# Optimization experiments

Measured on AMD Instinct MI355X. Metric: run time of the kernel, lower is better.

## Reference

```python
import jax, jax.numpy as jnp
import numpy as np

N_HEADS = 8
NEG_INF = -1e9


def setup_inputs() -> dict:
    key = jax.random.key(0)
    ks = jax.random.split(key, 9)
    B, S, D = 4, 2048, 512
    scale = 1.0 / np.sqrt(D)
    x = jax.random.normal(ks[0], (B, S, D), dtype=jnp.float32)
    mask = jnp.tril(jnp.ones((S, S), dtype=bool))[None, None, :, :]  # causal [1,1,S,S]
    W_Q_w = jax.random.normal(ks[1], (D, D), dtype=jnp.float32) * scale
    W_Q_b = jax.random.normal(ks[2], (D,), dtype=jnp.float32) * 0.02
    W_K_w = jax.random.normal(ks[3], (D, D), dtype=jnp.float32) * scale
    W_K_b = jax.random.normal(ks[4], (D,), dtype=jnp.float32) * 0.02
    W_V_w = jax.random.normal(ks[5], (D, D), dtype=jnp.float32) * scale
    W_V_b = jax.random.normal(ks[6], (D,), dtype=jnp.float32) * 0.02
    W_O_w = jax.random.normal(ks[7], (D, D), dtype=jnp.float32) * scale
    W_O_b = jax.random.normal(ks[8], (D,), dtype=jnp.float32) * 0.02
    return {"x": x, "mask": mask,
            "W_Q_w": W_Q_w, "W_Q_b": W_Q_b, "W_K_w": W_K_w, "W_K_b": W_K_b,
            "W_V_w": W_V_w, "W_V_b": W_V_b, "W_O_w": W_O_w, "W_O_b": W_O_b}


def reference(x, mask, W_Q_w, W_Q_b, W_K_w, W_K_b, W_V_w, W_V_b, W_O_w, W_O_b):
    B, S, D = x.shape
    H = N_HEADS
    Dh = D // H
    # projections (torch Linear: x @ W.T + b), split heads -> [B,H,S,Dh]
    def split_heads(t):
        return t.reshape(B, S, H, Dh).transpose(0, 2, 1, 3)
    Q = split_heads(x @ W_Q_w.T + W_Q_b)
    K = split_heads(x @ W_K_w.T + W_K_b)
    V = split_heads(x @ W_V_w.T + W_V_b)
    # scaled dot-product attention with explicit [B,H,S,S] scores
    scores = jnp.einsum("bhqd,bhkd->bhqk", Q, K) / jnp.sqrt(jnp.float32(Dh))
    scores = jnp.where(mask, scores, jnp.float32(NEG_INF))
    att = jax.nn.softmax(scores, axis=-1)
    out = jnp.einsum("bhqk,bhkd->bhqd", att, V)
    out = out.transpose(0, 2, 1, 3).reshape(B, S, D)
    return out @ W_O_w.T + W_O_b
```

## Files before the change

kernel.cpp:

```cpp
#include <hip/hip_runtime.h>
#include <hip/hip_bf16.h>

#define BATCH 4
#define SEQ   2048
#define DIM   512
#define NH    8
#define DH    64
#define NTOK  (BATCH*SEQ)

typedef __bf16 bf16x8 __attribute__((ext_vector_type(8)));
typedef __bf16 bf16x4 __attribute__((ext_vector_type(4)));
typedef float  f32x4  __attribute__((ext_vector_type(4)));

#define MFMA16(a,b,c) __builtin_amdgcn_mfma_f32_16x16x32_bf16((a),(b),(c),0,0,0)

__device__ __forceinline__ void async_ld16(const __bf16* g, __bf16* l) {
  __builtin_amdgcn_global_load_lds(
      (const __attribute__((address_space(1))) void*)g,
      (__attribute__((address_space(3))) void*)l, 16, 0, 0);
}

__global__ __launch_bounds__(256) void cvt_all(
    const float* __restrict__ x,
    const float* __restrict__ s0, const float* __restrict__ s1,
    const float* __restrict__ s2, const float* __restrict__ s3,
    __bf16* __restrict__ xb,
    __bf16* __restrict__ o0, __bf16* __restrict__ o1,
    __bf16* __restrict__ o2, __bf16* __restrict__ o3) {
  int i = blockIdx.x * blockDim.x + threadIdx.x;
  const float* src;
  __bf16* dst;
  int off;
  if (i < NTOK*DIM/8) {
    src = x; dst = xb; off = i;
  } else {
    int w = i - NTOK*DIM/8;
    const int which = w >> 15;
    off = w & 32767;
    src = (which == 0) ? s0 : (which == 1) ? s1 : (which == 2) ? s2 : s3;
    dst = (which == 0) ? o0 : (which == 1) ? o1 : (which == 2) ? o2 : o3;
  }
  const float4* s = (const float4*)src;
  float4 a = s[2*off], b = s[2*off+1];
  bf16x8 o;
  o[0] = (__bf16)a.x; o[1] = (__bf16)a.y; o[2] = (__bf16)a.z; o[3] = (__bf16)a.w;
  o[4] = (__bf16)b.x; o[5] = (__bf16)b.y; o[6] = (__bf16)b.z; o[7] = (__bf16)b.w;
  *(bf16x8*)&dst[8*off] = o;
}

__global__ __launch_bounds__(256) void gemm_qkv(
    const __bf16* __restrict__ xb,
    const __bf16* __restrict__ wq, const __bf16* __restrict__ wk,
    const __bf16* __restrict__ wv,
    const float* __restrict__ bq, const float* __restrict__ bk,
    const float* __restrict__ bv,
    __bf16* __restrict__ Qb, __bf16* __restrict__ Kb, __bf16* __restrict__ Vt)
{
  const int z = blockIdx.z;
  const __bf16* W    = (z == 0) ? wq : (z == 1) ? wk : wv;
  const float*  bias = (z == 0) ? bq : (z == 1) ? bk : bv;

  __shared__ __bf16 S[2][128*64];
  __bf16* As = S[0];
  __bf16* Bs = S[1];

  const int tid  = threadIdx.x;
  const int m0   = blockIdx.x * 128, n0 = blockIdx.y * 128;
  const int w    = tid >> 6, lane = tid & 63, quad = lane >> 4, l16 = lane & 15;
  const int wm   = (w >> 1) * 64, wn = (w & 1) * 64;
  const int lrow = lane >> 3;
  const int lcol = (lane & 7) * 8;

  f32x4 acc[4][4] = {};

  const __bf16* Ag = xb + (size_t)m0 * DIM;
  const __bf16* Bg = W  + (size_t)n0 * DIM;

  for (int k0 = 0; k0 < DIM; k0 += 64) {
#pragma unroll
    for (int i = 0; i < 4; ++i) {
      const int rb = w*32 + i*8;
      async_ld16(&Ag[(size_t)(rb + lrow)*DIM + k0 + lcol], &As[rb*64]);
      async_ld16(&Bg[(size_t)(rb + lrow)*DIM + k0 + lcol], &Bs[rb*64]);
    }
    __syncthreads();
#pragma unroll
    for (int kk = 0; kk < 2; ++kk) {
      const int ko = kk*32 + quad*8;
      bf16x8 af[4], bfr[4];
#pragma unroll
      for (int f = 0; f < 4; ++f) {
        af[f]  = *(const bf16x8*)&As[(wm + f*16 + l16)*64 + ko];
        bfr[f] = *(const bf16x8*)&Bs[(wn + f*16 + l16)*64 + ko];
      }
#pragma unroll
      for (int fm = 0; fm < 4; ++fm)
#pragma unroll
        for (int fn = 0; fn < 4; ++fn)
          acc[fm][fn] = MFMA16(af[fm], bfr[fn], acc[fm][fn]);
    }
    __syncthreads();
  }

  __bf16* Cs = &S[0][0];
  if (z < 2) {
#pragma unroll
    for (int fm = 0; fm < 4; ++fm)
#pragma unroll
      for (int fn = 0; fn < 4; ++fn) {
        const int col = wn + fn*16 + l16;
        const float bc = bias[n0 + col];
        const int chunk = col >> 3, ce = col & 7;
#pragma unroll
        for (int r = 0; r < 4; ++r) {
          const int row = wm + fm*16 + quad*4 + r;
          Cs[row*128 + ((chunk ^ (row & 7)) << 3) + ce] = (__bf16)(acc[fm][fn][r] + bc);
        }
      }
  } else {
#pragma unroll
    for (int fm = 0; fm < 4; ++fm)
#pragma unroll
      for (int fn = 0; fn < 4; ++fn) {
        const int dhcol = wn + fn*16 + l16;
        const float bc = bias[n0 + dhcol];
        const int sbase = wm + fm*16 + quad*4;
        const int schunk = sbase >> 3, so = sbase & 7;
        __bf16* p = &Cs[dhcol*128 + ((schunk ^ (dhcol & 7)) << 3) + so];
#pragma unroll
        for (int r = 0; r < 4; ++r)
          p[r] = (__bf16)(acc[fm][fn][r] + bc);
      }
  }
  __syncthreads();
  {
    const int row = tid >> 1, half = tid & 1;
    if (z < 2) {
      __bf16* O = (z == 0) ? Qb : Kb;
      const int s = m0 + row, bb = s >> 11, ss = s & 2047;
#pragma unroll
      for (int j = 0; j < 8; ++j) {
        const int chunk = half*8 + j;
        bf16x8 v = *(const bf16x8*)&Cs[row*128 + ((chunk ^ (row & 7)) << 3)];
        const int colg = n0 + chunk*8;
        const int hh = colg >> 6, dh = colg & 63;
        *(bf16x8*)&O[((size_t)(bb*NH + hh)*SEQ + ss)*DH + dh] = v;
      }
    } else {
      const int colg = n0 + row;
      const int hh = colg >> 6, dh = colg & 63;
      const int bb = m0 >> 11, s0s = m0 & 2047;
#pragma unroll
      for (int j = 0; j < 8; ++j) {
        const int chunk = half*8 + j;
        bf16x8 v = *(const bf16x8*)&Cs[row*128 + ((chunk ^ (row & 7)) << 3)];
        *(bf16x8*)&Vt[((size_t)(bb*NH + hh)*DH + dh)*SEQ + s0s + chunk*8] = v;
      }
    }
  }
}

__global__ __launch_bounds__(256) void gemm_out(
    const __bf16* __restrict__ attnb, const __bf16* __restrict__ wo,
    const float* __restrict__ bo, float* __restrict__ out)
{
  __shared__ __bf16 S[2][128*64];
  __bf16* As = S[0];
  __bf16* Bs = S[1];

  const int tid = threadIdx.x;
  const int m0  = blockIdx.x * 128, n0 = blockIdx.y * 128;
  const int w   = tid >> 6, lane = tid & 63, quad = lane >> 4, l16 = lane & 15;
  const int wm  = (w >> 1) * 64, wn = (w & 1) * 64;
  const int lrow = lane >> 3, lcol = (lane & 7) * 8;

  f32x4 acc[4][4] = {};

  const __bf16* Ag = attnb + (size_t)m0 * DIM;
  const __bf16* Bg = wo    + (size_t)n0 * DIM;

  for (int k0 = 0; k0 < DIM; k0 += 64) {
#pragma unroll
    for (int i = 0; i < 4; ++i) {
      const int rb = w*32 + i*8;
      async_ld16(&Ag[(size_t)(rb + lrow)*DIM + k0 + lcol], &As[rb*64]);
      async_ld16(&Bg[(size_t)(rb + lrow)*DIM + k0 + lcol], &Bs[rb*64]);
    }
    __syncthreads();
#pragma unroll
    for (int kk = 0; kk < 2; ++kk) {
      const int ko = kk*32 + quad*8;
      bf16x8 af[4], bfr[4];
#pragma unroll
      for (int f = 0; f < 4; ++f) {
        af[f]  = *(const bf16x8*)&As[(wm + f*16 + l16)*64 + ko];
        bfr[f] = *(const bf16x8*)&Bs[(wn + f*16 + l16)*64 + ko];
      }
#pragma unroll
      for (int fm = 0; fm < 4; ++fm)
#pragma unroll
        for (int fn = 0; fn < 4; ++fn)
          acc[fm][fn] = MFMA16(af[fm], bfr[fn], acc[fm][fn]);
    }
    __syncthreads();
  }

#pragma unroll
  for (int fm = 0; fm < 4; ++fm) {
#pragma unroll
    for (int fn = 0; fn < 4; ++fn) {
      const int col  = n0 + wn + fn*16 + l16;
      const float bc = bo[col];
#pragma unroll
      for (int r = 0; r < 4; ++r) {
        const int row = m0 + wm + fm*16 + quad*4 + r;
        out[(size_t)row*DIM + col] = acc[fm][fn][r] + bc;
      }
    }
  }
}

__global__ __launch_bounds__(64) void flash_attn(
    const __bf16* __restrict__ Qb, const __bf16* __restrict__ Kb,
    const __bf16* __restrict__ Vt, __bf16* __restrict__ attnb)
{
  const int idx = blockIdx.x;
  const int bh  = idx & 31;
  const int qt  = 63 - (idx >> 5);
  const int b   = bh >> 3, h = bh & 7;
  const int lane = threadIdx.x & 63, quad = lane >> 4, l16 = lane & 15;
  const int q0  = qt * 32;

  const __bf16* Qp = Qb + (size_t)bh * SEQ * DH;
  const __bf16* Kp = Kb + (size_t)bh * SEQ * DH;
  const __bf16* Vp = Vt + (size_t)bh * DH * SEQ;

  __shared__ __bf16 Pt[32*72];

  bf16x8 qf[2][2];
#pragma unroll
  for (int nf = 0; nf < 2; ++nf)
#pragma unroll
    for (int kc = 0; kc < 2; ++kc) {
      bf16x8 q = *(const bf16x8*)&Qp[(size_t)(q0 + nf*16 + l16)*DH + kc*32 + quad*8];
#pragma unroll
      for (int j = 0; j < 8; ++j) q[j] = (__bf16)((float)q[j] * 0.125f);
      qf[nf][kc] = q;
    }

  f32x4 o[4][2] = {};
  float m_[2] = {-1e30f, -1e30f}, l_[2] = {0.f, 0.f};

  const int nt = (q0 >> 6) + 1;

  bf16x8 kf[4][2];
  bf16x8 vf[4][2];
#pragma unroll
  for (int mf = 0; mf < 4; ++mf)
#pragma unroll
    for (int kc = 0; kc < 2; ++kc)
      kf[mf][kc] = *(const bf16x8*)&Kp[(size_t)(mf*16 + l16)*DH + kc*32 + quad*8];
#pragma unroll
  for (int df = 0; df < 4; ++df)
#pragma unroll
    for (int kc = 0; kc < 2; ++kc)
      vf[df][kc] = *(const bf16x8*)&Vp[(size_t)(df*16 + l16)*SEQ + kc*32 + quad*8];

  for (int kt = 0; kt < nt; ++kt) {
    const int k0 = kt * 64;
    const int kn0 = (kt + 1 < nt) ? k0 + 64 : k0;

    f32x4 s[4][2] = {};
#pragma unroll
    for (int mf = 0; mf < 4; ++mf)
#pragma unroll
      for (int nf = 0; nf < 2; ++nf) {
        s[mf][nf] = MFMA16(kf[mf][0], qf[nf][0], s[mf][nf]);
        s[mf][nf] = MFMA16(kf[mf][1], qf[nf][1], s[mf][nf]);
      }

#pragma unroll
    for (int mf = 0; mf < 4; ++mf)
#pragma unroll
      for (int kc = 0; kc < 2; ++kc)
        kf[mf][kc] = *(const bf16x8*)&Kp[(size_t)(kn0 + mf*16 + l16)*DH + kc*32 + quad*8];

    if (k0 + 63 > q0) {
#pragma unroll
      for (int nf = 0; nf < 2; ++nf) {
        const int q = q0 + nf*16 + l16;
#pragma unroll
        for (int mf = 0; mf < 4; ++mf) {
          const int kb = k0 + mf*16 + quad*4;
#pragma unroll
          for (int r = 0; r < 4; ++r)
            if (kb + r > q) s[mf][nf][r] = -1e30f;
        }
      }
    }

#pragma unroll
    for (int nf = 0; nf < 2; ++nf) {
      float mx = fmaxf(fmaxf(fmaxf(s[0][nf][0], s[0][nf][1]), fmaxf(s[0][nf][2], s[0][nf][3])),
                       fmaxf(fmaxf(s[1][nf][0], s[1][nf][1]), fmaxf(s[1][nf][2], s[1][nf][3])));
      float mx2 = fmaxf(fmaxf(fmaxf(s[2][nf][0], s[2][nf][1]), fmaxf(s[2][nf][2], s[2][nf][3])),
                        fmaxf(fmaxf(s[3][nf][0], s[3][nf][1]), fmaxf(s[3][nf][2], s[3][nf][3])));
      mx = fmaxf(mx, mx2);
      mx = fmaxf(mx, __shfl_xor(mx, 16));
      mx = fmaxf(mx, __shfl_xor(mx, 32));
      const float mn = fmaxf(m_[nf], mx);
      const float al = __expf(m_[nf] - mn);
      m_[nf] = mn;
      float sum = 0.f;
#pragma unroll
      for (int mf = 0; mf < 4; ++mf)
#pragma unroll
        for (int r = 0; r < 4; ++r) {
          const float e = __expf(s[mf][nf][r] - mn);
          s[mf][nf][r] = e;
          sum += e;
        }
      sum += __shfl_xor(sum, 16);
      sum += __shfl_xor(sum, 32);
      l_[nf] = l_[nf] * al + sum;
#pragma unroll
      for (int df = 0; df < 4; ++df)
#pragma unroll
        for (int r = 0; r < 4; ++r)
          o[df][nf][r] *= al;
    }

#pragma unroll
    for (int nf = 0; nf < 2; ++nf)
#pragma unroll
      for (int mf = 0; mf < 4; ++mf) {
        bf16x4 p4;
#pragma unroll
        for (int r = 0; r < 4; ++r) p4[r] = (__bf16)s[mf][nf][r];
        *(bf16x4*)&Pt[(nf*16 + l16)*72 + mf*16 + quad*4] = p4;
      }
    bf16x8 pb[2][2];
#pragma unroll
    for (int nf = 0; nf < 2; ++nf)
#pragma unroll
      for (int kc = 0; kc < 2; ++kc)
        pb[nf][kc] = *(const bf16x8*)&Pt[(nf*16 + l16)*72 + kc*32 + quad*8];

#pragma unroll
    for (int df = 0; df < 4; ++df)
#pragma unroll
      for (int nf = 0; nf < 2; ++nf) {
        o[df][nf] = MFMA16(vf[df][0], pb[nf][0], o[df][nf]);
        o[df][nf] = MFMA16(vf[df][1], pb[nf][1], o[df][nf]);
      }

#pragma unroll
    for (int df = 0; df < 4; ++df)
#pragma unroll
      for (int kc = 0; kc < 2; ++kc)
        vf[df][kc] = *(const bf16x8*)&Vp[(size_t)(df*16 + l16)*SEQ + kn0 + kc*32 + quad*8];
  }

#pragma unroll
  for (int nf = 0; nf < 2; ++nf) {
    const float inv = 1.0f / l_[nf];
    const int q = q0 + nf*16 + l16;
#pragma unroll
    for (int df = 0; df < 4; ++df) {
      bf16x4 o4;
#pragma unroll
      for (int r = 0; r < 4; ++r) o4[r] = (__bf16)(o[df][nf][r] * inv);
      *(bf16x4*)&attnb[((size_t)b*SEQ + q)*DIM + h*DH + df*16 + quad*4] = o4;
    }
  }
}

extern "C" void kernel_launch(void* const* d_in, const int* in_sizes, int n_in,
                              void* d_out, int out_size, void* d_ws, size_t ws_size,
                              hipStream_t stream) {
  const float* x  = (const float*)d_in[0];
  const float* Wq = (const float*)d_in[2];
  const float* bq = (const float*)d_in[3];
  const float* Wk = (const float*)d_in[4];
  const float* bk = (const float*)d_in[5];
  const float* Wv = (const float*)d_in[6];
  const float* bv = (const float*)d_in[7];
  const float* Wo = (const float*)d_in[8];
  const float* bo = (const float*)d_in[9];
  float* out = (float*)d_out;

  __bf16* xb    = (__bf16*)d_ws;
  __bf16* wq    = xb + (size_t)NTOK*DIM;
  __bf16* wk    = wq + DIM*DIM;
  __bf16* wv    = wk + DIM*DIM;
  __bf16* wo    = wv + DIM*DIM;
  __bf16* Qb    = wo + DIM*DIM;
  __bf16* Kb    = Qb + (size_t)NTOK*DIM;
  __bf16* Vt    = Kb + (size_t)NTOK*DIM;
  __bf16* attnb = Vt + (size_t)NTOK*DIM;

  cvt_all<<<(NTOK*DIM/8 + 4*DIM*DIM/8)/256, 256, 0, stream>>>(
      x, Wq, Wk, Wv, Wo, xb, wq, wk, wv, wo);

  gemm_qkv<<<dim3(NTOK/128, DIM/128, 3), 256, 0, stream>>>(
      xb, wq, wk, wv, bq, bk, bv, Qb, Kb, Vt);

  flash_attn<<<2048, 64, 0, stream>>>(Qb, Kb, Vt, attnb);

  gemm_out<<<dim3(NTOK/128, DIM/128), 256, 0, stream>>>(attnb, wo, bo, out);
}
```

Before: 215.6 us.

## Pair early and late query tiles per block to balance causal attention work

Each attention block now handles two 16-row query groups, one near the start of the sequence and one mirrored near the end, instead of one contiguous 32-row tile. The pairing gives every block about the same number of causal key tiles, which evens out the per-block work skew across the grid. It also switches the softmax to exp2 with log2(e) folded into the Q scaling. The cost is extra branching on whether the short group is still active, and the two groups share fewer key tiles, so the short group's key loads are not reused as fully as in a 32-row tile.

```diff
diff --git a/kernel.cpp b/kernel.cpp
--- a/kernel.cpp
+++ b/kernel.cpp
@@ -226,10 +226,13 @@
 {
   const int idx = blockIdx.x;
   const int bh  = idx & 31;
-  const int qt  = 63 - (idx >> 5);
+  const int j   = idx >> 5;
   const int b   = bh >> 3, h = bh & 7;
   const int lane = threadIdx.x & 63, quad = lane >> 4, l16 = lane & 15;
-  const int q0  = qt * 32;
+  const int q0A = j * 16;
+  const int q0B = (127 - j) * 16;
+  const int ntA = (q0A >> 6) + 1;
+  const int ntB = (q0B >> 6) + 1;
 
   const __bf16* Qp = Qb + (size_t)bh * SEQ * DH;
   const __bf16* Kp = Kb + (size_t)bh * SEQ * DH;
@@ -237,21 +240,22 @@
 
   __shared__ __bf16 Pt[32*72];
 
-  bf16x8 qf[2][2];
-#pragma unroll
-  for (int nf = 0; nf < 2; ++nf)
-#pragma unroll
-    for (int kc = 0; kc < 2; ++kc) {
-      bf16x8 q = *(const bf16x8*)&Qp[(size_t)(q0 + nf*16 + l16)*DH + kc*32 + quad*8];
-#pragma unroll
-      for (int j = 0; j < 8; ++j) q[j] = (__bf16)((float)q[j] * 0.125f);
-      qf[nf][kc] = q;
-    }
-
-  f32x4 o[4][2] = {};
-  float m_[2] = {-1e30f, -1e30f}, l_[2] = {0.f, 0.f};
-
-  const int nt = (q0 >> 6) + 1;
+  const float qs = 0.125f * 1.44269504088896f;
+  bf16x8 qfA[2], qfB[2];
+#pragma unroll
+  for (int kc = 0; kc < 2; ++kc) {
+    bf16x8 qa = *(const bf16x8*)&Qp[(size_t)(q0A + l16)*DH + kc*32 + quad*8];
+    bf16x8 qb = *(const bf16x8*)&Qp[(size_t)(q0B + l16)*DH + kc*32 + quad*8];
+#pragma unroll
+    for (int e = 0; e < 8; ++e) {
+      qa[e] = (__bf16)((float)qa[e] * qs);
+      qb[e] = (__bf16)((float)qb[e] * qs);
+    }
+    qfA[kc] = qa; qfB[kc] = qb;
+  }
+
+  f32x4 oA[4] = {}, oB[4] = {};
+  float mA = -1e30f, lA = 0.f, mB = -1e30f, lB = 0.f;
 
   bf16x8 kf[4][2];
   bf16x8 vf[4][2];
@@ -266,18 +270,58 @@
     for (int kc = 0; kc < 2; ++kc)
       vf[df][kc] = *(const bf16x8*)&Vp[(size_t)(df*16 + l16)*SEQ + kc*32 + quad*8];
 
-  for (int kt = 0; kt < nt; ++kt) {
+  auto softmax_update = [&](f32x4 (&s)[4], float& m_, float& l_, f32x4 (&o)[4]) {
+    float mx = fmaxf(fmaxf(fmaxf(s[0][0], s[0][1]), fmaxf(s[0][2], s[0][3])),
+                     fmaxf(fmaxf(s[1][0], s[1][1]), fmaxf(s[1][2], s[1][3])));
+    float mx2 = fmaxf(fmaxf(fmaxf(s[2][0], s[2][1]), fmaxf(s[2][2], s[2][3])),
+                      fmaxf(fmaxf(s[3][0], s[3][1]), fmaxf(s[3][2], s[3][3])));
+    mx = fmaxf(mx, mx2);
+    mx = fmaxf(mx, __shfl_xor(mx, 16));
+    mx = fmaxf(mx, __shfl_xor(mx, 32));
+    const float mn = fmaxf(m_, mx);
+    const float al = exp2f(m_ - mn);
+    m_ = mn;
+    float sum = 0.f;
+#pragma unroll
+    for (int mf = 0; mf < 4; ++mf)
+#pragma unroll
+      for (int r = 0; r < 4; ++r) {
+        const float e = exp2f(s[mf][r] - mn);
+        s[mf][r] = e;
+        sum += e;
+      }
+    sum += __shfl_xor(sum, 16);
+    sum += __shfl_xor(sum, 32);
+    l_ = l_ * al + sum;
+#pragma unroll
+    for (int df = 0; df < 4; ++df)
+#pragma unroll
+      for (int r = 0; r < 4; ++r)
+        o[df][r] *= al;
+  };
+
+  for (int kt = 0; kt < ntB; ++kt) {
     const int k0 = kt * 64;
-    const int kn0 = (kt + 1 < nt) ? k0 + 64 : k0;
-
-    f32x4 s[4][2] = {};
-#pragma unroll
-    for (int mf = 0; mf < 4; ++mf)
-#pragma unroll
-      for (int nf = 0; nf < 2; ++nf) {
-        s[mf][nf] = MFMA16(kf[mf][0], qf[nf][0], s[mf][nf]);
-        s[mf][nf] = MFMA16(kf[mf][1], qf[nf][1], s[mf][nf]);
-      }
+    const int kn0 = (kt + 1 < ntB) ? k0 + 64 : k0;
+    const bool doA = (kt < ntA);
+
+    f32x4 sA[4], sB[4];
+#pragma unroll
+    for (int mf = 0; mf < 4; ++mf) { sB[mf] = f32x4{}; }
+#pragma unroll
+    for (int mf = 0; mf < 4; ++mf) {
+      sB[mf] = MFMA16(kf[mf][0], qfB[0], sB[mf]);
+      sB[mf] = MFMA16(kf[mf][1], qfB[1], sB[mf]);
+    }
+    if (doA) {
+#pragma unroll
+      for (int mf = 0; mf < 4; ++mf) { sA[mf] = f32x4{}; }
+#pragma unroll
+      for (int mf = 0; mf < 4; ++mf) {
+        sA[mf] = MFMA16(kf[mf][0], qfA[0], sA[mf]);
+        sA[mf] = MFMA16(kf[mf][1], qfA[1], sA[mf]);
+      }
+    }
 
 #pragma unroll
     for (int mf = 0; mf < 4; ++mf)
@@ -285,74 +329,68 @@
       for (int kc = 0; kc < 2; ++kc)
         kf[mf][kc] = *(const bf16x8*)&Kp[(size_t)(kn0 + mf*16 + l16)*DH + kc*32 + quad*8];
 
-    if (k0 + 63 > q0) {
-#pragma unroll
-      for (int nf = 0; nf < 2; ++nf) {
-        const int q = q0 + nf*16 + l16;
-#pragma unroll
-        for (int mf = 0; mf < 4; ++mf) {
-          const int kb = k0 + mf*16 + quad*4;
-#pragma unroll
-          for (int r = 0; r < 4; ++r)
-            if (kb + r > q) s[mf][nf][r] = -1e30f;
-        }
-      }
-    }
-
-#pragma unroll
-    for (int nf = 0; nf < 2; ++nf) {
-      float mx = fmaxf(fmaxf(fmaxf(s[0][nf][0], s[0][nf][1]), fmaxf(s[0][nf][2], s[0][nf][3])),
-                       fmaxf(fmaxf(s[1][nf][0], s[1][nf][1]), fmaxf(s[1][nf][2], s[1][nf][3])));
-      float mx2 = fmaxf(fmaxf(fmaxf(s[2][nf][0], s[2][nf][1]), fmaxf(s[2][nf][2], s[2][nf][3])),
-                        fmaxf(fmaxf(s[3][nf][0], s[3][nf][1]), fmaxf(s[3][nf][2], s[3][nf][3])));
-      mx = fmaxf(mx, mx2);
-      mx = fmaxf(mx, __shfl_xor(mx, 16));
-      mx = fmaxf(mx, __shfl_xor(mx, 32));
-      const float mn = fmaxf(m_[nf], mx);
-      const float al = __expf(m_[nf] - mn);
-      m_[nf] = mn;
-      float sum = 0.f;
-#pragma unroll
-      for (int mf = 0; mf < 4; ++mf)
-#pragma unroll
-        for (int r = 0; r < 4; ++r) {
-          const float e = __expf(s[mf][nf][r] - mn);
-          s[mf][nf][r] = e;
-          sum += e;
-        }
-      sum += __shfl_xor(sum, 16);
-      sum += __shfl_xor(sum, 32);
-      l_[nf] = l_[nf] * al + sum;
-#pragma unroll
-      for (int df = 0; df < 4; ++df)
+    if (doA && (k0 + 63 > q0A)) {
+      const int q = q0A + l16;
+#pragma unroll
+      for (int mf = 0; mf < 4; ++mf) {
+        const int kb = k0 + mf*16 + quad*4;
 #pragma unroll
         for (int r = 0; r < 4; ++r)
-          o[df][nf][r] *= al;
-    }
-
-#pragma unroll
-    for (int nf = 0; nf < 2; ++nf)
+          if (kb + r > q) sA[mf][r] = -1e30f;
+      }
+    }
+    if (k0 + 63 > q0B) {
+      const int q = q0B + l16;
+#pragma unroll
+      for (int mf = 0; mf < 4; ++mf) {
+        const int kb = k0 + mf*16 + quad*4;
+#pragma unroll
+        for (int r = 0; r < 4; ++r)
+          if (kb + r > q) sB[mf][r] = -1e30f;
+      }
+    }
+
+    if (doA) softmax_update(sA, mA, lA, oA);
+    softmax_update(sB, mB, lB, oB);
+
+    if (doA) {
 #pragma unroll
       for (int mf = 0; mf < 4; ++mf) {
         bf16x4 p4;
 #pragma unroll
-        for (int r = 0; r < 4; ++r) p4[r] = (__bf16)s[mf][nf][r];
-        *(bf16x4*)&Pt[(nf*16 + l16)*72 + mf*16 + quad*4] = p4;
-      }
-    bf16x8 pb[2][2];
-#pragma unroll
-    for (int nf = 0; nf < 2; ++nf)
+        for (int r = 0; r < 4; ++r) p4[r] = (__bf16)sA[mf][r];
+        *(bf16x4*)&Pt[l16*72 + mf*16 + quad*4] = p4;
+      }
+    }
+#pragma unroll
+    for (int mf = 0; mf < 4; ++mf) {
+      bf16x4 p4;
+#pragma unroll
+      for (int r = 0; r < 4; ++r) p4[r] = (__bf16)sB[mf][r];
+      *(bf16x4*)&Pt[(16 + l16)*72 + mf*16 + quad*4] = p4;
+    }
+    bf16x8 pbA[2], pbB[2];
+    if (doA) {
 #pragma unroll
       for (int kc = 0; kc < 2; ++kc)
-        pb[nf][kc] = *(const bf16x8*)&Pt[(nf*16 + l16)*72 + kc*32 + quad*8];
-
-#pragma unroll
-    for (int df = 0; df < 4; ++df)
-#pragma unroll
-      for (int nf = 0; nf < 2; ++nf) {
-        o[df][nf] = MFMA16(vf[df][0], pb[nf][0], o[df][nf]);
-        o[df][nf] = MFMA16(vf[df][1], pb[nf][1], o[df][nf]);
-      }
+        pbA[kc] = *(const bf16x8*)&Pt[l16*72 + kc*32 + quad*8];
+    }
+#pragma unroll
+    for (int kc = 0; kc < 2; ++kc)
+      pbB[kc] = *(const bf16x8*)&Pt[(16 + l16)*72 + kc*32 + quad*8];
+
+#pragma unroll
+    for (int df = 0; df < 4; ++df) {
+      oB[df] = MFMA16(vf[df][0], pbB[0], oB[df]);
+      oB[df] = MFMA16(vf[df][1], pbB[1], oB[df]);
+    }
+    if (doA) {
+#pragma unroll
+      for (int df = 0; df < 4; ++df) {
+        oA[df] = MFMA16(vf[df][0], pbA[0], oA[df]);
+        oA[df] = MFMA16(vf[df][1], pbA[1], oA[df]);
+      }
+    }
 
 #pragma unroll
     for (int df = 0; df < 4; ++df)
@@ -361,18 +399,19 @@
         vf[df][kc] = *(const bf16x8*)&Vp[(size_t)(df*16 + l16)*SEQ + kn0 + kc*32 + quad*8];
   }
 
-#pragma unroll
-  for (int nf = 0; nf < 2; ++nf) {
-    const float inv = 1.0f / l_[nf];
-    const int q = q0 + nf*16 + l16;
+  auto store_group = [&](f32x4 (&o)[4], float l_, int q0) {
+    const float inv = 1.0f / l_;
+    const int q = q0 + l16;
 #pragma unroll
     for (int df = 0; df < 4; ++df) {
       bf16x4 o4;
 #pragma unroll
-      for (int r = 0; r < 4; ++r) o4[r] = (__bf16)(o[df][nf][r] * inv);
+      for (int r = 0; r < 4; ++r) o4[r] = (__bf16)(o[df][r] * inv);
       *(bf16x4*)&attnb[((size_t)b*SEQ + q)*DIM + h*DH + df*16 + quad*4] = o4;
     }
-  }
+  };
+  store_group(oA, lA, q0A);
+  store_group(oB, lB, q0B);
 }
 
 extern "C" void kernel_launch(void* const* d_in, const int* in_sizes, int n_in,
```

Measured after the change: 238.1 us. 1.1x slower.

## Shrink flash-attention query tile to 16 and software-pipeline QK^T across key tiles

Applied to the files above, without the earlier changes.

The attention kernel now assigns 16 query rows per single-wave block instead of 32, doubling the grid to 4096 blocks for more parallelism and finer causal load balance. The QK^T MFMA for the next key tile is issued before softmax of the current tile, using ping-pong score buffers in a two-step unrolled loop, so matrix work overlaps softmax latency. Scores are pre-scaled by log2(e) so softmax uses exp2f. The cost is twice as many K/V reads per query row, since each block rereads the full causal K/V prefix for only 16 queries.

```diff
diff --git a/kernel.cpp b/kernel.cpp
--- a/kernel.cpp
+++ b/kernel.cpp
@@ -226,32 +226,30 @@
 {
   const int idx = blockIdx.x;
   const int bh  = idx & 31;
-  const int qt  = 63 - (idx >> 5);
+  const int qt  = 127 - (idx >> 5);
   const int b   = bh >> 3, h = bh & 7;
   const int lane = threadIdx.x & 63, quad = lane >> 4, l16 = lane & 15;
-  const int q0  = qt * 32;
+  const int q0  = qt * 16;
+  const int nt  = (q0 >> 6) + 1;
 
   const __bf16* Qp = Qb + (size_t)bh * SEQ * DH;
   const __bf16* Kp = Kb + (size_t)bh * SEQ * DH;
   const __bf16* Vp = Vt + (size_t)bh * DH * SEQ;
 
-  __shared__ __bf16 Pt[32*72];
-
-  bf16x8 qf[2][2];
-#pragma unroll
-  for (int nf = 0; nf < 2; ++nf)
-#pragma unroll
-    for (int kc = 0; kc < 2; ++kc) {
-      bf16x8 q = *(const bf16x8*)&Qp[(size_t)(q0 + nf*16 + l16)*DH + kc*32 + quad*8];
-#pragma unroll
-      for (int j = 0; j < 8; ++j) q[j] = (__bf16)((float)q[j] * 0.125f);
-      qf[nf][kc] = q;
-    }
-
-  f32x4 o[4][2] = {};
-  float m_[2] = {-1e30f, -1e30f}, l_[2] = {0.f, 0.f};
-
-  const int nt = (q0 >> 6) + 1;
+  __shared__ __bf16 Pt[16*72];
+
+  const float qs = 0.125f * 1.4426950408889634f;
+  bf16x8 qf[2];
+#pragma unroll
+  for (int kc = 0; kc < 2; ++kc) {
+    bf16x8 q = *(const bf16x8*)&Qp[(size_t)(q0 + l16)*DH + kc*32 + quad*8];
+#pragma unroll
+    for (int e = 0; e < 8; ++e) q[e] = (__bf16)((float)q[e] * qs);
+    qf[kc] = q;
+  }
+
+  f32x4 o[4] = {};
+  float m_ = -1e30f, l_ = 0.f;
 
   bf16x8 kf[4][2];
   bf16x8 vf[4][2];
@@ -266,110 +264,129 @@
     for (int kc = 0; kc < 2; ++kc)
       vf[df][kc] = *(const bf16x8*)&Vp[(size_t)(df*16 + l16)*SEQ + kc*32 + quad*8];
 
-  for (int kt = 0; kt < nt; ++kt) {
-    const int k0 = kt * 64;
-    const int kn0 = (kt + 1 < nt) ? k0 + 64 : k0;
-
-    f32x4 s[4][2] = {};
+  f32x4 sA[4], sB[4];
+#pragma unroll
+  for (int mf = 0; mf < 4; ++mf) {
+    sA[mf] = f32x4{};
+    sA[mf] = MFMA16(kf[mf][0], qf[0], sA[mf]);
+    sA[mf] = MFMA16(kf[mf][1], qf[1], sA[mf]);
+  }
+  {
+    const int kn = (nt > 1) ? 64 : 0;
 #pragma unroll
     for (int mf = 0; mf < 4; ++mf)
 #pragma unroll
-      for (int nf = 0; nf < 2; ++nf) {
-        s[mf][nf] = MFMA16(kf[mf][0], qf[nf][0], s[mf][nf]);
-        s[mf][nf] = MFMA16(kf[mf][1], qf[nf][1], s[mf][nf]);
-      }
-
-#pragma unroll
-    for (int mf = 0; mf < 4; ++mf)
-#pragma unroll
       for (int kc = 0; kc < 2; ++kc)
-        kf[mf][kc] = *(const bf16x8*)&Kp[(size_t)(kn0 + mf*16 + l16)*DH + kc*32 + quad*8];
-
-    if (k0 + 63 > q0) {
-#pragma unroll
-      for (int nf = 0; nf < 2; ++nf) {
-        const int q = q0 + nf*16 + l16;
-#pragma unroll
-        for (int mf = 0; mf < 4; ++mf) {
-          const int kb = k0 + mf*16 + quad*4;
-#pragma unroll
-          for (int r = 0; r < 4; ++r)
-            if (kb + r > q) s[mf][nf][r] = -1e30f;
-        }
-      }
-    }
-
-#pragma unroll
-    for (int nf = 0; nf < 2; ++nf) {
-      float mx = fmaxf(fmaxf(fmaxf(s[0][nf][0], s[0][nf][1]), fmaxf(s[0][nf][2], s[0][nf][3])),
-                       fmaxf(fmaxf(s[1][nf][0], s[1][nf][1]), fmaxf(s[1][nf][2], s[1][nf][3])));
-      float mx2 = fmaxf(fmaxf(fmaxf(s[2][nf][0], s[2][nf][1]), fmaxf(s[2][nf][2], s[2][nf][3])),
-                        fmaxf(fmaxf(s[3][nf][0], s[3][nf][1]), fmaxf(s[3][nf][2], s[3][nf][3])));
-      mx = fmaxf(mx, mx2);
-      mx = fmaxf(mx, __shfl_xor(mx, 16));
-      mx = fmaxf(mx, __shfl_xor(mx, 32));
-      const float mn = fmaxf(m_[nf], mx);
-      const float al = __expf(m_[nf] - mn);
-      m_[nf] = mn;
-      float sum = 0.f;
-#pragma unroll
-      for (int mf = 0; mf < 4; ++mf)
-#pragma unroll
-        for (int r = 0; r < 4; ++r) {
-          const float e = __expf(s[mf][nf][r] - mn);
-          s[mf][nf][r] = e;
-          sum += e;
-        }
-      sum += __shfl_xor(sum, 16);
-      sum += __shfl_xor(sum, 32);
-      l_[nf] = l_[nf] * al + sum;
-#pragma unroll
-      for (int df = 0; df < 4; ++df)
-#pragma unroll
-        for (int r = 0; r < 4; ++r)
-          o[df][nf][r] *= al;
-    }
-
-#pragma unroll
-    for (int nf = 0; nf < 2; ++nf)
-#pragma unroll
-      for (int mf = 0; mf < 4; ++mf) {
-        bf16x4 p4;
-#pragma unroll
-        for (int r = 0; r < 4; ++r) p4[r] = (__bf16)s[mf][nf][r];
-        *(bf16x4*)&Pt[(nf*16 + l16)*72 + mf*16 + quad*4] = p4;
-      }
-    bf16x8 pb[2][2];
-#pragma unroll
-    for (int nf = 0; nf < 2; ++nf)
-#pragma unroll
-      for (int kc = 0; kc < 2; ++kc)
-        pb[nf][kc] = *(const bf16x8*)&Pt[(nf*16 + l16)*72 + kc*32 + quad*8];
-
-#pragma unroll
-    for (int df = 0; df < 4; ++df)
-#pragma unroll
-      for (int nf = 0; nf < 2; ++nf) {
-        o[df][nf] = MFMA16(vf[df][0], pb[nf][0], o[df][nf]);
-        o[df][nf] = MFMA16(vf[df][1], pb[nf][1], o[df][nf]);
-      }
-
-#pragma unroll
-    for (int df = 0; df < 4; ++df)
-#pragma unroll
-      for (int kc = 0; kc < 2; ++kc)
-        vf[df][kc] = *(const bf16x8*)&Vp[(size_t)(df*16 + l16)*SEQ + kn0 + kc*32 + quad*8];
-  }
-
-#pragma unroll
-  for (int nf = 0; nf < 2; ++nf) {
-    const float inv = 1.0f / l_[nf];
-    const int q = q0 + nf*16 + l16;
+        kf[mf][kc] = *(const bf16x8*)&Kp[(size_t)(kn + mf*16 + l16)*DH + kc*32 + quad*8];
+  }
+
+#define PSTEP(SC, SN, KT)                                                      \
+  {                                                                            \
+    const int k0 = (KT) * 64;                                                  \
+    const bool hasNext = ((KT) + 1 < nt);                                      \
+    if (hasNext) {                                                             \
+      _Pragma("unroll")                                                        \
+      for (int mf = 0; mf < 4; ++mf) {                                         \
+        SN[mf] = f32x4{};                                                      \
+        SN[mf] = MFMA16(kf[mf][0], qf[0], SN[mf]);                             \
+        SN[mf] = MFMA16(kf[mf][1], qf[1], SN[mf]);                             \
+      }                                                                        \
+      const int kn2 = ((KT) + 2 < nt) ? k0 + 128 : k0;                         \
+      _Pragma("unroll")                                                        \
+      for (int mf = 0; mf < 4; ++mf)                                           \
+        _Pragma("unroll")                                                      \
+        for (int kc = 0; kc < 2; ++kc)                                         \
+          kf[mf][kc] = *(const bf16x8*)&Kp[(size_t)(kn2 + mf*16 + l16)*DH +    \
+                                           kc*32 + quad*8];                    \
+    }                                                                          \
+    if (k0 + 63 > q0) {                                                        \
+      const int q = q0 + l16;                                                  \
+      _Pragma("unroll")                                                        \
+      for (int mf = 0; mf < 4; ++mf) {                                         \
+        const int kb = k0 + mf*16 + quad*4;                                    \
+        _Pragma("unroll")                                                      \
+        for (int r = 0; r < 4; ++r)                                            \
+          if (kb + r > q) SC[mf][r] = -1e30f;                                  \
+      }                                                                        \
+    }                                                                          \
+                                        \
+    {                                                                          \
+      float mx = fmaxf(fmaxf(fmaxf(SC[0][0], SC[0][1]),                        \
+                             fmaxf(SC[0][2], SC[0][3])),                       \
+                       fmaxf(fmaxf(SC[1][0], SC[1][1]),                        \
+                             fmaxf(SC[1][2], SC[1][3])));                      \
+      float mx2 = fmaxf(fmaxf(fmaxf(SC[2][0], SC[2][1]),                       \
+                              fmaxf(SC[2][2], SC[2][3])),                      \
+                        fmaxf(fmaxf(SC[3][0], SC[3][1]),                       \
+                              fmaxf(SC[3][2], SC[3][3])));                     \
+      mx = fmaxf(mx, mx2);                                                     \
+      mx = fmaxf(mx, __shfl_xor(mx, 16));                                      \
+      mx = fmaxf(mx, __shfl_xor(mx, 32));                                      \
+      const float mn = fmaxf(m_, mx);                                          \
+      const float al = exp2f(m_ - mn);                                         \
+      m_ = mn;                                                                 \
+      float sum = 0.f;                                                         \
+      _Pragma("unroll")                                                        \
+      for (int mf = 0; mf < 4; ++mf)                                           \
+        _Pragma("unroll")                                                      \
+        for (int r = 0; r < 4; ++r) {                                          \
+          const float e = exp2f(SC[mf][r] - mn);                               \
+          SC[mf][r] = e;                                                       \
+          sum += e;                                                            \
+        }                                                                      \
+      sum += __shfl_xor(sum, 16);                                              \
+      sum += __shfl_xor(sum, 32);                                              \
+      l_ = l_ * al + sum;                                                      \
+      _Pragma("unroll")                                                        \
+      for (int df = 0; df < 4; ++df)                                           \
+        _Pragma("unroll")                                                      \
+        for (int r = 0; r < 4; ++r)                                            \
+          o[df][r] *= al;                                                      \
+    }                                                                          \
+                                       \
+    _Pragma("unroll")                                                          \
+    for (int mf = 0; mf < 4; ++mf) {                                           \
+      bf16x4 p4;                                                               \
+      _Pragma("unroll")                                                        \
+      for (int r = 0; r < 4; ++r) p4[r] = (__bf16)SC[mf][r];                   \
+      *(bf16x4*)&Pt[l16*72 + mf*16 + quad*4] = p4;                             \
+    }                                                                          \
+    bf16x8 pb[2];                                                              \
+    _Pragma("unroll")                                                          \
+    for (int kc = 0; kc < 2; ++kc)                                             \
+      pb[kc] = *(const bf16x8*)&Pt[l16*72 + kc*32 + quad*8];                   \
+                                                           \
+    _Pragma("unroll")                                                          \
+    for (int df = 0; df < 4; ++df) {                                           \
+      o[df] = MFMA16(vf[df][0], pb[0], o[df]);                                 \
+      o[df] = MFMA16(vf[df][1], pb[1], o[df]);                                 \
+    }                                                                          \
+                                                     \
+    {                                                                          \
+      const int kv = hasNext ? k0 + 64 : k0;                                   \
+      _Pragma("unroll")                                                        \
+      for (int df = 0; df < 4; ++df)                                           \
+        _Pragma("unroll")                                                      \
+        for (int kc = 0; kc < 2; ++kc)                                         \
+          vf[df][kc] = *(const bf16x8*)&Vp[(size_t)(df*16 + l16)*SEQ + kv +    \
+                                           kc*32 + quad*8];                    \
+    }                                                                          \
+  }
+
+  for (int kt = 0; kt < nt; kt += 2) {
+    PSTEP(sA, sB, kt);
+    if (kt + 1 < nt) PSTEP(sB, sA, kt + 1);
+  }
+#undef PSTEP
+
+  {
+    const float inv = 1.0f / l_;
+    const int q = q0 + l16;
 #pragma unroll
     for (int df = 0; df < 4; ++df) {
       bf16x4 o4;
 #pragma unroll
-      for (int r = 0; r < 4; ++r) o4[r] = (__bf16)(o[df][nf][r] * inv);
+      for (int r = 0; r < 4; ++r) o4[r] = (__bf16)(o[df][r] * inv);
       *(bf16x4*)&attnb[((size_t)b*SEQ + q)*DIM + h*DH + df*16 + quad*4] = o4;
     }
   }
@@ -405,7 +422,7 @@
   gemm_qkv<<<dim3(NTOK/128, DIM/128, 3), 256, 0, stream>>>(
       xb, wq, wk, wv, bq, bk, bv, Qb, Kb, Vt);
 
-  flash_attn<<<2048, 64, 0, stream>>>(Qb, Kb, Vt, attnb);
+  flash_attn<<<4096, 64, 0, stream>>>(Qb, Kb, Vt, attnb);
 
   gemm_out<<<dim3(NTOK/128, DIM/128), 256, 0, stream>>>(attnb, wo, bo, out);
 }
```

Measured after the change: 271.7 us. +26.0%, slower.
